# Kernel tuning notes

Hardware: AMD Instinct MI355X
Metric: run time of the kernel (lower is better)

The kernel has to match this reference:

```python
import jax, jax.numpy as jnp
import numpy as np

NIN, NOUT = 256, 64

def setup_inputs() -> dict:
    key = jax.random.key(0)
    k1, k2, k3, k4 = jax.random.split(key, 4)
    B, T = 4, 4096
    y = jax.random.normal(k1, (B, T, NIN), dtype=jnp.float32)
    # torch Linear(nin, nout).weight has shape [nout, nin]; store as [nin, nout]
    s = 1.0 / np.sqrt(NIN)
    Wq = jax.random.uniform(k2, (NIN, NOUT), jnp.float32, -s, s)
    Wk = jax.random.uniform(k3, (NIN, NOUT), jnp.float32, -s, s)
    Wv = jax.random.uniform(k4, (NIN, NOUT), jnp.float32, -s, s)
    return {"y": y, "Wq": Wq, "Wk": Wk, "Wv": Wv}

def reference(y, Wq, Wk, Wv):
    T = y.shape[1]
    que = y @ Wq  # [B,T,NOUT]
    key = y @ Wk
    val = y @ Wv
    att = jnp.einsum('bqd,bkd->bqk', que, key)  # [B,T,T]
    causal = jnp.tril(jnp.ones((T, T), dtype=bool))  # True = keep
    att = jnp.where(causal, att, -jnp.inf)
    att = jax.nn.softmax(att / jnp.sqrt(jnp.float32(NOUT)), axis=-1)
    return jnp.einsum('bqk,bkd->bqd', att, val)
```

## Files before the change

### kernel.cpp

```cpp
#include <hip/hip_runtime.h>
#include <hip/hip_bf16.h>

#define TLEN 4096
#define NINP 256
#define DD   64

#define QSCALE 0.18033688011112042f

typedef __attribute__((ext_vector_type(8))) short bf16x8;
typedef __attribute__((ext_vector_type(4))) short bf16x4;
typedef __attribute__((ext_vector_type(4))) float f32x4;

union U8 { bf16x8 v; uint u[4]; };
union U4 { bf16x4 v; uint u[2]; };

__device__ inline ushort bfu(float x) {
    union { float f; uint u; } a; a.f = x;
    uint r = a.u + 0x7fffu + ((a.u >> 16) & 1u);
    return (ushort)(r >> 16);
}
__device__ inline uint pk2(float lo, float hi) {
    return (uint)bfu(lo) | ((uint)bfu(hi) << 16);
}

__device__ inline bf16x8 ld16(const ushort* p) {
    return *(const bf16x8*)p;
}
__device__ inline bf16x8 ld8x2(const ushort* p) {
    U8 u;
    uint2 a = *(const uint2*)p;
    uint2 b = *(const uint2*)(p + 4);
    u.u[0] = a.x; u.u[1] = a.y; u.u[2] = b.x; u.u[3] = b.y;
    return u.v;
}

__global__ __launch_bounds__(256) void prep_wt(
    const float* __restrict__ Wq, const float* __restrict__ Wk,
    const float* __restrict__ Wv, ushort* __restrict__ WT)
{
    __shared__ ushort lt[256 * 66];
    const int t = threadIdx.x;
    const int m = blockIdx.x;
    const float* W = (m == 0) ? Wq : ((m == 1) ? Wk : Wv);
    const float scale = (m == 0) ? QSCALE : 1.0f;

    #pragma unroll
    for (int j = 0; j < 16; ++j) {
        int i4 = t + 256 * j;
        float4 v = *(const float4*)&W[i4 * 4];
        int k = i4 >> 4, d = (i4 * 4) & 63;
        *(uint*)&lt[k * 66 + d]     = pk2(v.x * scale, v.y * scale);
        *(uint*)&lt[k * 66 + d + 2] = pk2(v.z * scale, v.w * scale);
    }
    __syncthreads();
    #pragma unroll
    for (int j = 0; j < 32; ++j) {
        int o2 = t + 256 * j;
        int d = o2 >> 7, k = (o2 & 127) * 2;
        uint pk = (uint)lt[k * 66 + d] | ((uint)lt[(k + 1) * 66 + d] << 16);
        *(uint*)&WT[m * 16384 + d * 256 + k] = pk;
    }
}

__global__ __launch_bounds__(256, 3) void qkv_kernel(
    const float* __restrict__ y, const ushort* __restrict__ WT,
    ushort* __restrict__ Qh, ushort* __restrict__ Kp, ushort* __restrict__ Vp,
    const int rbn)
{
    __shared__ ushort Wl[64 * 268];
    __shared__ ushort tb[64 * 68];

    const int t = threadIdx.x;
    const int w = t >> 6, lane = t & 63;
    const int quad = lane >> 4, l15 = lane & 15;
    const int mb = blockIdx.x / rbn;
    const int rb = blockIdx.x % rbn;
    const int rowbase = rb * 64;
    const int myrow = rowbase + w * 16 + l15;

    {
        int n = t >> 2, seg = t & 3;
        const ushort* src = WT + mb * 16384 + n * 256 + seg * 64;
        ushort* dst = &Wl[n * 268 + seg * 64];
        #pragma unroll
        for (int j = 0; j < 16; ++j)
            ((uint2*)dst)[j] = ((const uint2*)src)[j];
    }

    bf16x8 afrag[8];
    const float* yrow = y + (size_t)myrow * NINP;
    #pragma unroll
    for (int s = 0; s < 8; ++s) {
        float4 lo = *(const float4*)&yrow[s * 32 + quad * 8];
        float4 hi = *(const float4*)&yrow[s * 32 + quad * 8 + 4];
        U8 u;
        u.u[0] = pk2(lo.x, lo.y);
        u.u[1] = pk2(lo.z, lo.w);
        u.u[2] = pk2(hi.x, hi.y);
        u.u[3] = pk2(hi.z, hi.w);
        afrag[s] = u.v;
    }

    __syncthreads();

    f32x4 acc[4];
    #pragma unroll
    for (int nt = 0; nt < 4; ++nt) acc[nt] = f32x4{0.f, 0.f, 0.f, 0.f};

    #pragma unroll
    for (int s = 0; s < 8; ++s)
        #pragma unroll
        for (int nt = 0; nt < 4; ++nt) {
            bf16x8 bfrag = ld8x2(&Wl[(nt * 16 + l15) * 268 + s * 32 + quad * 8]);
            acc[nt] = __builtin_amdgcn_mfma_f32_16x16x32_bf16(
                afrag[s], bfrag, acc[nt], 0, 0, 0);
        }

    if (mb == 0) {
        #pragma unroll
        for (int nt = 0; nt < 4; ++nt)
            #pragma unroll
            for (int r = 0; r < 4; ++r)
                tb[(w * 16 + quad * 4 + r) * 68 + nt * 16 + l15] = bfu(acc[nt][r]);
        __syncthreads();
        int row = t >> 2, seg = t & 3;
        ushort* gd = Qh + (size_t)(rowbase + row) * DD + seg * 16;
        const ushort* sp = &tb[row * 68 + seg * 16];
        #pragma unroll
        for (int j = 0; j < 4; ++j) ((uint2*)gd)[j] = ((const uint2*)sp)[j];
    } else if (mb == 1) {
        #pragma unroll
        for (int nt = 0; nt < 4; ++nt)
            #pragma unroll
            for (int r = 0; r < 4; ++r)
                tb[(w * 16 + quad * 4 + r) * 68 + nt * 16 + l15] = bfu(acc[nt][r]);
        __syncthreads();
        #pragma unroll
        for (int j = 0; j < 2; ++j) {
            int idx = t + 256 * j;
            int instr = idx >> 6, ln = idx & 63;
            int kt = instr >> 1, s = instr & 1;
            int q2 = ln >> 4, l15b = ln & 15;
            int row = kt * 16 + l15b, dcol = s * 32 + q2 * 8;
            const ushort* sp = &tb[row * 68 + dcol];
            ushort* gd = Kp + (size_t)rb * 4096 + idx * 8;
            ((uint2*)gd)[0] = ((const uint2*)sp)[0];
            ((uint2*)gd)[1] = ((const uint2*)sp)[1];
        }
    } else {
        #pragma unroll
        for (int nt = 0; nt < 4; ++nt) {
            int d = nt * 16 + l15;
            #pragma unroll
            for (int r = 0; r < 4; r += 2) {
                int tt = w * 16 + quad * 4 + r;
                *(uint*)&tb[d * 68 + tt] = pk2(acc[nt][r], acc[nt][r + 1]);
            }
        }
        __syncthreads();
        #pragma unroll
        for (int j = 0; j < 2; ++j) {
            int idx = t + 256 * j;
            int instr = idx >> 6, ln = idx & 63;
            int nt = instr >> 1, m = instr & 1;
            int q2 = ln >> 4, l15b = ln & 15;
            int d = nt * 16 + l15b;
            int k0 = 32 * m + q2 * 4;
            ushort* gd = Vp + (size_t)rb * 4096 + idx * 8;
            ((uint2*)gd)[0] = *(const uint2*)&tb[d * 68 + k0];
            ((uint2*)gd)[1] = *(const uint2*)&tb[d * 68 + k0 + 16];
        }
    }
}

__device__ inline void load_k(bf16x8 (&kf)[4][2], const ushort* __restrict__ Kpb,
                              int ci, int lane)
{
    const ushort* base = Kpb + (size_t)ci * 4096 + lane * 8;
    #pragma unroll
    for (int kt = 0; kt < 4; ++kt)
        #pragma unroll
        for (int s = 0; s < 2; ++s)
            kf[kt][s] = ld16(base + (kt * 2 + s) * 512);
}

__device__ inline void load_v(U4 (&vt)[4][4], const ushort* __restrict__ Vpb,
                              int ci, int lane)
{
    const ushort* base = Vpb + (size_t)ci * 4096 + lane * 8;
    #pragma unroll
    for (int nt = 0; nt < 4; ++nt)
        #pragma unroll
        for (int m = 0; m < 2; ++m) {
            U8 uu; uu.v = ld16(base + (nt * 2 + m) * 512);
            vt[nt][2 * m].u[0]     = uu.u[0];
            vt[nt][2 * m].u[1]     = uu.u[1];
            vt[nt][2 * m + 1].u[0] = uu.u[2];
            vt[nt][2 * m + 1].u[1] = uu.u[3];
        }
}

__global__ __launch_bounds__(512, 2) void attn_kernel(
    const ushort* __restrict__ Qh, const ushort* __restrict__ Kp,
    const ushort* __restrict__ Vp, float* __restrict__ out)
{
    __shared__ float Ob[8][32 * 68];
    __shared__ float lb[8][32];

    const int t = threadIdx.x;
    const int w = t >> 6, lane = t & 63;
    const int quad = lane >> 4, l15 = lane & 15;

    const int x  = blockIdx.x & 7;
    const int b  = x >> 1;
    const int r_ = (int)blockIdx.x >> 3;
    const int h  = r_ >> 5;
    const int j0 = ((r_ & 31) << 1) | (x & 1);
    const int tile = h ? (127 - j0) : j0;

    const int seg = w;
    const int qb  = tile * 32;
    const int nc  = (tile + 2) >> 1;
    const int cps = (nc + 7) >> 3;
    const int clo = seg * cps;
    const int chi = (nc < clo + cps) ? nc : (clo + cps);

    const ushort* Qb  = Qh + (size_t)b * TLEN * DD;
    const ushort* Kpb = Kp + (size_t)b * 64 * 4096;
    const ushort* Vpb = Vp + (size_t)b * 64 * 4096;
    float* outb = out + (size_t)b * TLEN * DD;

    f32x4 oT[2][4];
    #pragma unroll
    for (int qt = 0; qt < 2; ++qt)
        #pragma unroll
        for (int nt = 0; nt < 4; ++nt)
            oT[qt][nt] = f32x4{0.f, 0.f, 0.f, 0.f};
    float l_acc[2] = {0.f, 0.f};

    if (clo < chi) {
        bf16x8 qf[2][2];
        #pragma unroll
        for (int qt = 0; qt < 2; ++qt)
            #pragma unroll
            for (int s = 0; s < 2; ++s)
                qf[qt][s] = ld16(Qb + (size_t)(qb + qt * 16 + l15) * DD + s * 32 + quad * 8);

        bf16x8 kf[4][2];
        load_k(kf, Kpb, clo, lane);

        for (int ci = clo; ci < chi; ++ci) {
            const int c0 = ci * 64;

            U4 vt[4][4];
            load_v(vt, Vpb, ci, lane);

            f32x4 st[2][4];
            #pragma unroll
            for (int qt = 0; qt < 2; ++qt)
                #pragma unroll
                for (int kt = 0; kt < 4; ++kt)
                    st[qt][kt] = f32x4{0.f, 0.f, 0.f, 0.f};
            __builtin_amdgcn_s_setprio(1);
            #pragma unroll
            for (int s = 0; s < 2; ++s)
                #pragma unroll
                for (int qt = 0; qt < 2; ++qt)
                    #pragma unroll
                    for (int kt = 0; kt < 4; ++kt)
                        st[qt][kt] = __builtin_amdgcn_mfma_f32_16x16x32_bf16(
                            kf[kt][s], qf[qt][s], st[qt][kt], 0, 0, 0);
            __builtin_amdgcn_s_setprio(0);

            if (ci + 1 < chi) load_k(kf, Kpb, ci + 1, lane);

            U4 pa[2][4];
            if (c0 + 63 <= qb) {
                #pragma unroll
                for (int qt = 0; qt < 2; ++qt)
                    #pragma unroll
                    for (int kt = 0; kt < 4; ++kt) {
                        float p0 = exp2f(st[qt][kt][0]);
                        float p1 = exp2f(st[qt][kt][1]);
                        float p2 = exp2f(st[qt][kt][2]);
                        float p3 = exp2f(st[qt][kt][3]);
                        l_acc[qt] += (p0 + p1) + (p2 + p3);
                        pa[qt][kt].u[0] = pk2(p0, p1);
                        pa[qt][kt].u[1] = pk2(p2, p3);
                    }
            } else {
                #pragma unroll
                for (int qt = 0; qt < 2; ++qt) {
                    const int q = qb + qt * 16 + l15;
                    #pragma unroll
                    for (int kt = 0; kt < 4; ++kt) {
                        const int kb0 = c0 + kt * 16 + quad * 4;
                        float p[4];
                        #pragma unroll
                        for (int r = 0; r < 4; ++r) {
                            float e = exp2f(st[qt][kt][r]);
                            p[r] = (kb0 + r <= q) ? e : 0.f;
                            l_acc[qt] += p[r];
                        }
                        pa[qt][kt].u[0] = pk2(p[0], p[1]);
                        pa[qt][kt].u[1] = pk2(p[2], p[3]);
                    }
                }
            }

            __builtin_amdgcn_s_setprio(1);
            #pragma unroll
            for (int qt = 0; qt < 2; ++qt)
                #pragma unroll
                for (int nt = 0; nt < 4; ++nt)
                    #pragma unroll
                    for (int kt = 0; kt < 4; ++kt)
                        oT[qt][nt] = __builtin_amdgcn_mfma_f32_16x16x16bf16_1k(
                            vt[nt][kt].v, pa[qt][kt].v, oT[qt][nt], 0, 0, 0);
            __builtin_amdgcn_s_setprio(0);
        }

        #pragma unroll
        for (int qt = 0; qt < 2; ++qt) {
            l_acc[qt] += __shfl_xor(l_acc[qt], 16, 64);
            l_acc[qt] += __shfl_xor(l_acc[qt], 32, 64);
        }
    }

    #pragma unroll
    for (int qt = 0; qt < 2; ++qt) {
        #pragma unroll
        for (int nt = 0; nt < 4; ++nt)
            #pragma unroll
            for (int r = 0; r < 4; ++r)
                Ob[w][(qt * 16 + l15) * 68 + nt * 16 + quad * 4 + r] = oT[qt][nt][r];
        if (quad == 0) lb[w][qt * 16 + l15] = l_acc[qt];
    }
    __syncthreads();

    #pragma unroll
    for (int e = 0; e < 4; ++e) {
        int idx = t + 512 * e;
        int q = idx >> 6, d = idx & 63;
        float s = 0.f, ls = 0.f;
        #pragma unroll
        for (int ww = 0; ww < 8; ++ww) {
            s += Ob[ww][q * 68 + d];
            ls += lb[ww][q];
        }
        outb[(size_t)(qb + q) * DD + d] = s * __builtin_amdgcn_rcpf(ls);
    }
}

extern "C" void kernel_launch(void* const* d_in, const int* in_sizes, int n_in,
                              void* d_out, int out_size, void* d_ws, size_t ws_size,
                              hipStream_t stream) {
    const float* y  = (const float*)d_in[0];
    const float* Wq = (const float*)d_in[1];
    const float* Wk = (const float*)d_in[2];
    const float* Wv = (const float*)d_in[3];
    float* outp = (float*)d_out;

    const int rows = in_sizes[0] / NINP;
    const int rbn = rows / 64;

    ushort* WT = (ushort*)d_ws;
    ushort* Qh = WT + 3 * 16384;
    ushort* Kp = Qh + (size_t)rows * DD;
    ushort* Vp = Kp + (size_t)rows * DD;

    prep_wt<<<3, 256, 0, stream>>>(Wq, Wk, Wv, WT);
    qkv_kernel<<<3 * rbn, 256, 0, stream>>>(y, WT, Qh, Kp, Vp, rbn);
    attn_kernel<<<rbn * 2, 512, 0, stream>>>(Qh, Kp, Vp, outp);
}
```

Before: 103.4 us.

## Halve key chunk size to 32 and raise occupancy to four blocks per CU

The attention inner loop now processes 32-key chunks instead of 64, which halves the K/V fragment and score registers per iteration. The launch bounds go from 2 to 4 blocks per multiprocessor to use the freed registers. Finer chunks also reduce wasted masked work on the causal diagonal and balance the per-wave key splits better. The cost is more loop iterations and loads per key, and shared memory may limit whether the higher occupancy can actually be reached.

```diff
diff --git a/kernel.cpp b/kernel.cpp
--- a/kernel.cpp
+++ b/kernel.cpp
@@ -173,34 +173,30 @@
     }
 }
 
-__device__ inline void load_k(bf16x8 (&kf)[4][2], const ushort* __restrict__ Kpb,
-                              int ci, int lane)
-{
-    const ushort* base = Kpb + (size_t)ci * 4096 + lane * 8;
-    #pragma unroll
-    for (int kt = 0; kt < 4; ++kt)
+__device__ inline void load_k32(bf16x8 (&kf)[2][2], const ushort* __restrict__ Kw,
+                                int ci)
+{
+    const ushort* base = Kw + (size_t)ci * 2048;
+    #pragma unroll
+    for (int kt = 0; kt < 2; ++kt)
         #pragma unroll
         for (int s = 0; s < 2; ++s)
             kf[kt][s] = ld16(base + (kt * 2 + s) * 512);
 }
 
-__device__ inline void load_v(U4 (&vt)[4][4], const ushort* __restrict__ Vpb,
-                              int ci, int lane)
-{
-    const ushort* base = Vpb + (size_t)ci * 4096 + lane * 8;
-    #pragma unroll
-    for (int nt = 0; nt < 4; ++nt)
-        #pragma unroll
-        for (int m = 0; m < 2; ++m) {
-            U8 uu; uu.v = ld16(base + (nt * 2 + m) * 512);
-            vt[nt][2 * m].u[0]     = uu.u[0];
-            vt[nt][2 * m].u[1]     = uu.u[1];
-            vt[nt][2 * m + 1].u[0] = uu.u[2];
-            vt[nt][2 * m + 1].u[1] = uu.u[3];
-        }
-}
-
-__global__ __launch_bounds__(512, 2) void attn_kernel(
+__device__ inline void load_v32(U4 (&vt)[4][2], const ushort* __restrict__ Vw,
+                                int ci)
+{
+    const ushort* base = Vw + (size_t)(ci >> 1) * 4096 + (ci & 1) * 512;
+    #pragma unroll
+    for (int nt = 0; nt < 4; ++nt) {
+        U8 uu; uu.v = ld16(base + nt * 1024);
+        vt[nt][0].u[0] = uu.u[0]; vt[nt][0].u[1] = uu.u[1];
+        vt[nt][1].u[0] = uu.u[2]; vt[nt][1].u[1] = uu.u[3];
+    }
+}
+
+__global__ __launch_bounds__(512, 4) void attn_kernel(
     const ushort* __restrict__ Qh, const ushort* __restrict__ Kp,
     const ushort* __restrict__ Vp, float* __restrict__ out)
 {
@@ -220,14 +216,14 @@
 
     const int seg = w;
     const int qb  = tile * 32;
-    const int nc  = (tile + 2) >> 1;
+    const int nc  = tile + 1;
     const int cps = (nc + 7) >> 3;
     const int clo = seg * cps;
     const int chi = (nc < clo + cps) ? nc : (clo + cps);
 
-    const ushort* Qb  = Qh + (size_t)b * TLEN * DD;
-    const ushort* Kpb = Kp + (size_t)b * 64 * 4096;
-    const ushort* Vpb = Vp + (size_t)b * 64 * 4096;
+    const ushort* Qb = Qh + (size_t)b * TLEN * DD;
+    const ushort* Kw = Kp + (size_t)b * 64 * 4096 + lane * 8;
+    const ushort* Vw = Vp + (size_t)b * 64 * 4096 + lane * 8;
     float* outb = out + (size_t)b * TLEN * DD;
 
     f32x4 oT[2][4];
@@ -246,20 +242,20 @@
             for (int s = 0; s < 2; ++s)
                 qf[qt][s] = ld16(Qb + (size_t)(qb + qt * 16 + l15) * DD + s * 32 + quad * 8);
 
-        bf16x8 kf[4][2];
-        load_k(kf, Kpb, clo, lane);
+        bf16x8 kf[2][2];
+        load_k32(kf, Kw, clo);
 
         for (int ci = clo; ci < chi; ++ci) {
-            const int c0 = ci * 64;
-
-            U4 vt[4][4];
-            load_v(vt, Vpb, ci, lane);
-
-            f32x4 st[2][4];
+            const int c0 = ci * 32;
+
+            U4 vt[4][2];
+            load_v32(vt, Vw, ci);
+
+            f32x4 st[2][2];
             #pragma unroll
             for (int qt = 0; qt < 2; ++qt)
                 #pragma unroll
-                for (int kt = 0; kt < 4; ++kt)
+                for (int kt = 0; kt < 2; ++kt)
                     st[qt][kt] = f32x4{0.f, 0.f, 0.f, 0.f};
             __builtin_amdgcn_s_setprio(1);
             #pragma unroll
@@ -267,19 +263,19 @@
                 #pragma unroll
                 for (int qt = 0; qt < 2; ++qt)
                     #pragma unroll
-                    for (int kt = 0; kt < 4; ++kt)
+                    for (int kt = 0; kt < 2; ++kt)
                         st[qt][kt] = __builtin_amdgcn_mfma_f32_16x16x32_bf16(
                             kf[kt][s], qf[qt][s], st[qt][kt], 0, 0, 0);
             __builtin_amdgcn_s_setprio(0);
 
-            if (ci + 1 < chi) load_k(kf, Kpb, ci + 1, lane);
-
-            U4 pa[2][4];
-            if (c0 + 63 <= qb) {
+            if (ci + 1 < chi) load_k32(kf, Kw, ci + 1);
+
+            U4 pa[2][2];
+            if (c0 + 31 <= qb) {
                 #pragma unroll
                 for (int qt = 0; qt < 2; ++qt)
                     #pragma unroll
-                    for (int kt = 0; kt < 4; ++kt) {
+                    for (int kt = 0; kt < 2; ++kt) {
                         float p0 = exp2f(st[qt][kt][0]);
                         float p1 = exp2f(st[qt][kt][1]);
                         float p2 = exp2f(st[qt][kt][2]);
@@ -293,7 +289,7 @@
                 for (int qt = 0; qt < 2; ++qt) {
                     const int q = qb + qt * 16 + l15;
                     #pragma unroll
-                    for (int kt = 0; kt < 4; ++kt) {
+                    for (int kt = 0; kt < 2; ++kt) {
                         const int kb0 = c0 + kt * 16 + quad * 4;
                         float p[4];
                         #pragma unroll
@@ -314,7 +310,7 @@
                 #pragma unroll
                 for (int nt = 0; nt < 4; ++nt)
                     #pragma unroll
-                    for (int kt = 0; kt < 4; ++kt)
+                    for (int kt = 0; kt < 2; ++kt)
                         oT[qt][nt] = __builtin_amdgcn_mfma_f32_16x16x16bf16_1k(
                             vt[nt][kt].v, pa[qt][kt].v, oT[qt][nt], 0, 0, 0);
             __builtin_amdgcn_s_setprio(0);
```

Result: no change. 103.3 us (-0.1%).
